# Performance work log

Hardware: AMD Instinct MI355X
Metric: run time of the kernel (lower is better)

## Reference

```python
import jax, jax.numpy as jnp
import numpy as np

B, T, D, H, O, E = 4, 2048, 1024, 2048, 1024, 8
EPS = 1e-12  # torch F.normalize p=1 eps


def setup_inputs() -> dict:
    key = jax.random.key(0)
    ks = jax.random.split(key, 8)
    s = lambda *dims: 1.0 / np.sqrt(dims[0])
    return {
        "x": jax.random.normal(ks[0], (B, T, D), dtype=jnp.float32),
        "num_experts_chosen": 2,
        "W_gate": jax.random.normal(ks[1], (D, E), dtype=jnp.float32) * s(D),
        "b_gate": jnp.zeros((E,), dtype=jnp.float32),
        "W1": jax.random.normal(ks[2], (E, D, H), dtype=jnp.float32) * s(D),
        "b1": jnp.zeros((E, H), dtype=jnp.float32),
        "W2": jax.random.normal(ks[3], (E, H, O), dtype=jnp.float32) * s(H),
        "b2": jnp.zeros((E, O), dtype=jnp.float32),
    }


def reference(x, num_experts_chosen, W_gate, b_gate, W1, b1, W2, b2):
    # Router: softmax over experts -> [b, t, E]
    gating = jax.nn.softmax(jnp.einsum("btd,de->bte", x, W_gate) + b_gate, axis=-1)

    # Top-k mask (scatter of ones at top-k indices), then L1 renormalize
    _, topk_idx = jax.lax.top_k(gating, num_experts_chosen)  # [b, t, k]
    mask = jax.nn.one_hot(topk_idx, E, dtype=gating.dtype).sum(axis=-2)  # [b, t, E]
    g = gating * mask
    g = g / jnp.maximum(jnp.sum(jnp.abs(g), axis=-1, keepdims=True), EPS)

    # Dense compute of ALL experts (faithful to original), eval-mode dropout = identity
    h = jax.nn.relu(jnp.einsum("btd,edh->bteh", x, W1) + b1)  # [b, t, E, H]
    eo = jnp.einsum("bteh,eho->bteo", h, W2) + b2              # [b, t, E, O]

    # Weighted combine over experts
    return jnp.einsum("bte,bteo->bto", g, eo)
```

## Files before the change

### kernel.cpp

```cpp
#include <hip/hip_runtime.h>
#include <hip/hip_bf16.h>

typedef unsigned short u16;
typedef __attribute__((ext_vector_type(8))) short short8;
typedef __attribute__((ext_vector_type(4))) float floatx4;

#define NB 4
#define NT 2048
#define ND 1024
#define NH 2048
#define NO 1024
#define NE 8
#define NTOK (NB * NT)

#define BM 128
#define BN 128
#define BK 32

__device__ __forceinline__ u16 f2bf(float f) {
  __hip_bfloat16 h = __float2bfloat16(f);
  return *reinterpret_cast<u16*>(&h);
}

__device__ __forceinline__ float bf2f(unsigned u) {
  return __uint_as_float(u << 16);
}

__device__ __forceinline__ void async16(const u16* g, u16* l) {
  __builtin_amdgcn_global_load_lds(
      (const __attribute__((address_space(1))) void*)g,
      (__attribute__((address_space(3))) void*)l, 16, 0, 0);
}

__global__ __launch_bounds__(256) void transpose_cvt(
    const float* __restrict__ in, u16* __restrict__ out, int R, int C) {
  __shared__ float tile[64][65];
  int e = blockIdx.z;
  in  += (size_t)e * R * C;
  out += (size_t)e * R * C;
  int c0 = blockIdx.x * 64, r0 = blockIdx.y * 64;
  int t = threadIdx.x;
#pragma unroll
  for (int i = 0; i < 4; ++i) {
    int idx = t + i * 256;
    int r = idx >> 4, cq = idx & 15;
    float4 v = *(const float4*)&in[(size_t)(r0 + r) * C + c0 + cq * 4];
    tile[r][cq * 4 + 0] = v.x; tile[r][cq * 4 + 1] = v.y;
    tile[r][cq * 4 + 2] = v.z; tile[r][cq * 4 + 3] = v.w;
  }
  __syncthreads();
#pragma unroll
  for (int i = 0; i < 4; ++i) {
    int idx = t + i * 256;
    int c = idx >> 4, rq = idx & 15;
    uint2 p;
    p.x = (unsigned)f2bf(tile[rq * 4 + 0][c]) | ((unsigned)f2bf(tile[rq * 4 + 1][c]) << 16);
    p.y = (unsigned)f2bf(tile[rq * 4 + 2][c]) | ((unsigned)f2bf(tile[rq * 4 + 3][c]) << 16);
    *(uint2*)&out[(size_t)(c0 + c) * R + r0 + rq * 4] = p;
  }
}

__global__ __launch_bounds__(256) void router_kernel(
    const float* __restrict__ x, const float* __restrict__ Wg,
    const float* __restrict__ bg, u16* __restrict__ xbf,
    int* __restrict__ counts, int* __restrict__ entries,
    float* __restrict__ wts) {
  __shared__ int   se0[32], se1[32];
  __shared__ float sw0[32], sw1[32];
  int t = threadIdx.x;
  int tl = t >> 3;
  int l8 = t & 7;
  int tok = blockIdx.x * 32 + tl;

  const float* xrow = x + (size_t)tok * ND;
  u16* xbrow = xbf + (size_t)tok * ND;
  float acc[8] = {};
#pragma unroll 4
  for (int i = 0; i < 32; ++i) {
    int d0 = l8 * 4 + i * 32;
    float4 xv = *(const float4*)&xrow[d0];
    uint2 p;
    p.x = (unsigned)f2bf(xv.x) | ((unsigned)f2bf(xv.y) << 16);
    p.y = (unsigned)f2bf(xv.z) | ((unsigned)f2bf(xv.w) << 16);
    *(uint2*)&xbrow[d0] = p;
    const float* wr = Wg + (size_t)d0 * NE;
#pragma unroll
    for (int j = 0; j < 4; ++j) {
      float xs = (j == 0) ? xv.x : (j == 1) ? xv.y : (j == 2) ? xv.z : xv.w;
      float4 w0 = *(const float4*)&wr[j * NE];
      float4 w1 = *(const float4*)&wr[j * NE + 4];
      acc[0] += xs * w0.x; acc[1] += xs * w0.y;
      acc[2] += xs * w0.z; acc[3] += xs * w0.w;
      acc[4] += xs * w1.x; acc[5] += xs * w1.y;
      acc[6] += xs * w1.z; acc[7] += xs * w1.w;
    }
  }
#pragma unroll
  for (int off = 4; off; off >>= 1)
#pragma unroll
    for (int k = 0; k < 8; ++k) acc[k] += __shfl_down(acc[k], off, 8);

  if (l8 == 0) {
    float best = -1e30f, second = -1e30f;
    int e0 = 0, e1 = 0;
#pragma unroll
    for (int i = 0; i < NE; ++i) {
      float L = acc[i] + bg[i];
      if (L > best) { second = best; e1 = e0; best = L; e0 = i; }
      else if (L > second) { second = L; e1 = i; }
    }
    float p1 = __expf(second - best);
    float inv = 1.f / (1.f + p1);
    se0[tl] = e0; se1[tl] = e1;
    sw0[tl] = inv; sw1[tl] = p1 * inv;
  }
  __syncthreads();

  if (t < NE) {
    int e = t;
    int c = 0;
#pragma unroll
    for (int k = 0; k < 32; ++k) c += (se0[k] == e) + (se1[k] == e);
    int pos = atomicAdd(&counts[e * 32], c);
    int base = blockIdx.x * 32;
    for (int k = 0; k < 32; ++k) {
      if (se0[k] == e) { entries[e * NTOK + pos] = (base + k) * 2;     wts[e * NTOK + pos] = sw0[k]; ++pos; }
      if (se1[k] == e) { entries[e * NTOK + pos] = (base + k) * 2 + 1; wts[e * NTOK + pos] = sw1[k]; ++pos; }
    }
  }
}

__global__ __launch_bounds__(256) void gemm1_kernel(
    const u16* __restrict__ xbf, const u16* __restrict__ w1t,
    const float* __restrict__ b1, const int* __restrict__ counts,
    const int* __restrict__ entries, u16* __restrict__ hbuf) {
  int b = blockIdx.x;
  int e = b & 7;
  int r = b >> 3;
  int mIdx = r >> 4;
  int n0 = (r & 15) * BN;
  int cnt = counts[e * 32];

  __shared__ u16 As[BM * BK];
  __shared__ u16 Bs[BN * BK];
  __shared__ int ent_s[BM];

  int t = threadIdx.x;
  int lane = t & 63, wv = t >> 6;
  int rl0 = wv * 32 + (lane >> 2);
  int rl1 = rl0 + 16;
  int pg = (((lane & 3) ^ ((rl0 >> 1) & 3))) * 8;
  const u16* Bbase = w1t + (size_t)e * NH * ND + (size_t)n0 * ND;
  const u16* gB0 = Bbase + (size_t)rl0 * ND + pg;
  const u16* gB1 = Bbase + (size_t)rl1 * ND + pg;
  u16* lA0 = As + (wv * 32) * BK;
  u16* lA1 = As + (wv * 32 + 16) * BK;
  u16* lB0 = Bs + (wv * 32) * BK;
  u16* lB1 = Bs + (wv * 32 + 16) * BK;

  int waveM = (wv >> 1) * 64, waveN = (wv & 1) * 64;
  int rA = lane & 15, quad = lane >> 4;
  int cR = (quad ^ ((rA >> 1) & 3)) * 8;
  const short8* aP[4]; const short8* bP[4];
#pragma unroll
  for (int i = 0; i < 4; ++i) {
    aP[i] = (const short8*)&As[(waveM + i * 16 + rA) * BK + cR];
    bP[i] = (const short8*)&Bs[(waveN + i * 16 + rA) * BK + cR];
  }

  for (int m0 = mIdx * BM; m0 < cnt; m0 += 16 * BM) {
    int rem = cnt - m0; if (rem > BM) rem = BM;
    if (t < BM) ent_s[t] = (t < rem) ? entries[e * NTOK + m0 + t] : entries[e * NTOK];
    __syncthreads();

    const u16* gA0 = xbf + (size_t)(ent_s[rl0] >> 1) * ND + pg;
    const u16* gA1 = xbf + (size_t)(ent_s[rl1] >> 1) * ND + pg;

    floatx4 acc[4][4] = {};
    for (int k0 = 0; k0 < ND; k0 += BK) {
      async16(gA0 + k0, lA0);
      async16(gA1 + k0, lA1);
      async16(gB0 + k0, lB0);
      async16(gB1 + k0, lB1);
      __syncthreads();
      short8 a[4], bb[4];
#pragma unroll
      for (int i = 0; i < 4; ++i) { a[i] = *aP[i]; bb[i] = *bP[i]; }
#pragma unroll
      for (int i = 0; i < 4; ++i)
#pragma unroll
        for (int j = 0; j < 4; ++j)
          acc[i][j] = __builtin_amdgcn_mfma_f32_16x16x32_bf16(a[i], bb[j], acc[i][j], 0, 0, 0);
      __syncthreads();
    }

#pragma unroll
    for (int i = 0; i < 4; ++i)
#pragma unroll
      for (int rr = 0; rr < 4; ++rr) {
        int lm = waveM + i * 16 + quad * 4 + rr;
        if (lm >= rem) continue;
        int ent = ent_s[lm];
        u16* dst = hbuf + (size_t)ent * NH + n0;
#pragma unroll
        for (int j = 0; j < 4; ++j) {
          int col = waveN + j * 16 + rA;
          float v = acc[i][j][rr] + b1[e * NH + n0 + col];
          dst[col] = f2bf(fmaxf(v, 0.f));
        }
      }
    __syncthreads();
  }
}

__global__ __launch_bounds__(256) void gemm2_kernel(
    const u16* __restrict__ hbuf, const u16* __restrict__ w2t,
    const float* __restrict__ b2, const int* __restrict__ counts,
    const int* __restrict__ entries, const float* __restrict__ wts,
    u16* __restrict__ eo) {
  int b = blockIdx.x;
  int e = b & 7;
  int r = b >> 3;
  int mIdx = r >> 3;
  int n0 = (r & 7) * BN;
  int cnt = counts[e * 32];

  __shared__ u16 As[BM * BK];
  __shared__ u16 Bs[BN * BK];
  __shared__ int ent_s[BM];
  __shared__ float w_s[BM];

  int t = threadIdx.x;
  int lane = t & 63, wv = t >> 6;
  int rl0 = wv * 32 + (lane >> 2);
  int rl1 = rl0 + 16;
  int pg = (((lane & 3) ^ ((rl0 >> 1) & 3))) * 8;
  const u16* Bbase = w2t + (size_t)e * NO * NH + (size_t)n0 * NH;
  const u16* gB0 = Bbase + (size_t)rl0 * NH + pg;
  const u16* gB1 = Bbase + (size_t)rl1 * NH + pg;
  u16* lA0 = As + (wv * 32) * BK;
  u16* lA1 = As + (wv * 32 + 16) * BK;
  u16* lB0 = Bs + (wv * 32) * BK;
  u16* lB1 = Bs + (wv * 32 + 16) * BK;

  int waveM = (wv >> 1) * 64, waveN = (wv & 1) * 64;
  int rA = lane & 15, quad = lane >> 4;
  int cR = (quad ^ ((rA >> 1) & 3)) * 8;
  const short8* aP[4]; const short8* bP[4];
#pragma unroll
  for (int i = 0; i < 4; ++i) {
    aP[i] = (const short8*)&As[(waveM + i * 16 + rA) * BK + cR];
    bP[i] = (const short8*)&Bs[(waveN + i * 16 + rA) * BK + cR];
  }

  for (int m0 = mIdx * BM; m0 < cnt; m0 += 16 * BM) {
    int rem = cnt - m0; if (rem > BM) rem = BM;
    if (t < BM) {
      int src = (t < rem) ? (e * NTOK + m0 + t) : (e * NTOK);
      ent_s[t] = entries[src];
      w_s[t] = wts[src];
    }
    __syncthreads();

    const u16* gA0 = hbuf + (size_t)ent_s[rl0] * NH + pg;
    const u16* gA1 = hbuf + (size_t)ent_s[rl1] * NH + pg;

    floatx4 acc[4][4] = {};
    for (int k0 = 0; k0 < NH; k0 += BK) {
      async16(gA0 + k0, lA0);
      async16(gA1 + k0, lA1);
      async16(gB0 + k0, lB0);
      async16(gB1 + k0, lB1);
      __syncthreads();
      short8 a[4], bb[4];
#pragma unroll
      for (int i = 0; i < 4; ++i) { a[i] = *aP[i]; bb[i] = *bP[i]; }
#pragma unroll
      for (int i = 0; i < 4; ++i)
#pragma unroll
        for (int j = 0; j < 4; ++j)
          acc[i][j] = __builtin_amdgcn_mfma_f32_16x16x32_bf16(a[i], bb[j], acc[i][j], 0, 0, 0);
      __syncthreads();
    }

#pragma unroll
    for (int i = 0; i < 4; ++i)
#pragma unroll
      for (int rr = 0; rr < 4; ++rr) {
        int lm = waveM + i * 16 + quad * 4 + rr;
        if (lm >= rem) continue;
        int ent = ent_s[lm];
        float w = w_s[lm];
        u16* dst = eo + (size_t)ent * NO + n0;
#pragma unroll
        for (int j = 0; j < 4; ++j) {
          int col = waveN + j * 16 + rA;
          float v = (acc[i][j][rr] + b2[e * NO + n0 + col]) * w;
          dst[col] = f2bf(v);
        }
      }
    __syncthreads();
  }
}

__global__ __launch_bounds__(256) void combine_kernel(
    const u16* __restrict__ eo, float* __restrict__ out) {
  size_t idx = (size_t)blockIdx.x * 256 + threadIdx.x;
  size_t tok = idx >> 8;
  int oq = (int)(idx & 255) * 4;
  const u16* p0 = eo + (tok * 2) * NO + oq;
  const u16* p1 = p0 + NO;
  uint2 ua = *(const uint2*)p0;
  uint2 ub = *(const uint2*)p1;
  float4 o;
  o.x = bf2f(ua.x & 0xffff) + bf2f(ub.x & 0xffff);
  o.y = bf2f(ua.x >> 16)    + bf2f(ub.x >> 16);
  o.z = bf2f(ua.y & 0xffff) + bf2f(ub.y & 0xffff);
  o.w = bf2f(ua.y >> 16)    + bf2f(ub.y >> 16);
  *(float4*)&out[tok * NO + oq] = o;
}

extern "C" void kernel_launch(void* const* d_in, const int* in_sizes, int n_in,
                              void* d_out, int out_size, void* d_ws, size_t ws_size,
                              hipStream_t stream) {
  (void)in_sizes; (void)n_in; (void)out_size; (void)ws_size;
  const float* x  = (const float*)d_in[0];
  const float* Wg = (const float*)d_in[2];
  const float* bg = (const float*)d_in[3];
  const float* W1 = (const float*)d_in[4];
  const float* b1 = (const float*)d_in[5];
  const float* W2 = (const float*)d_in[6];
  const float* b2 = (const float*)d_in[7];
  float* out = (float*)d_out;

  char* ws = (char*)d_ws;
  size_t off = 0;
  int*   counts  = (int*)(ws + off);   off += NE * 32 * 4;
  int*   entries = (int*)(ws + off);   off += (size_t)NE * NTOK * 4;
  float* wts     = (float*)(ws + off); off += (size_t)NE * NTOK * 4;
  u16*   xbf     = (u16*)(ws + off);   off += (size_t)NTOK * ND * 2;
  u16*   w1t     = (u16*)(ws + off);   off += (size_t)NE * NH * ND * 2;
  u16*   w2t     = (u16*)(ws + off);   off += (size_t)NE * NO * NH * 2;
  u16*   hbuf    = (u16*)(ws + off);   off += (size_t)NTOK * 2 * NH * 2;
  u16*   eo      = w1t;

  hipMemsetAsync(counts, 0, NE * 32 * 4, stream);

  transpose_cvt<<<dim3(NH / 64, ND / 64, NE), 256, 0, stream>>>(W1, w1t, ND, NH);
  transpose_cvt<<<dim3(NO / 64, NH / 64, NE), 256, 0, stream>>>(W2, w2t, NH, NO);
  router_kernel<<<NTOK / 32, 256, 0, stream>>>(x, Wg, bg, xbf, counts, entries, wts);
  gemm1_kernel<<<NE * 16 * (NH / BN), 256, 0, stream>>>(xbf, w1t, b1, counts, entries, hbuf);
  gemm2_kernel<<<NE * 16 * (NO / BN), 256, 0, stream>>>(hbuf, w2t, b2, counts, entries, wts, eo);
  combine_kernel<<<(NTOK * NO / 4) / 256, 256, 0, stream>>>(eo, out);
}
```

Baseline: 502.9 us.

## Double GEMM K-tile to 64 with 8-way LDS swizzle and fuse prep kernels

Raises BK from 32 to 64 in both expert GEMMs. Each k-step now loads four 16-byte async chunks per operand per thread and issues two MFMA k-substeps, which halves the number of barrier pairs per tile. It also changes the LDS XOR swizzle to 8 chunks to match the wider rows. Separately, the router and both weight transpose/convert kernels are merged into one prep kernel launch so they can overlap and launch overhead drops. The cost is double the LDS per block, which may lower occupancy, and a larger shared tile allocation in every prep block.

After: 456.8 us. -9.2%, faster.

```diff
diff --git a/kernel.cpp b/kernel.cpp
--- a/kernel.cpp
+++ b/kernel.cpp
@@ -15,7 +15,11 @@
 
 #define BM 128
 #define BN 128
-#define BK 32
+#define BK 64
+
+#define RTR_BLKS (NTOK / 32)
+#define T1_BLKS  ((NH / 64) * (ND / 64) * NE)
+#define T2_BLKS  ((NO / 64) * (NH / 64) * NE)
 
 __device__ __forceinline__ u16 f2bf(float f) {
   __hip_bfloat16 h = __float2bfloat16(f);
@@ -32,13 +36,12 @@
       (__attribute__((address_space(3))) void*)l, 16, 0, 0);
 }
 
-__global__ __launch_bounds__(256) void transpose_cvt(
-    const float* __restrict__ in, u16* __restrict__ out, int R, int C) {
-  __shared__ float tile[64][65];
-  int e = blockIdx.z;
+__device__ __forceinline__ void transpose_body(
+    const float* __restrict__ in, u16* __restrict__ out, int R, int C,
+    int bx, int by, int e, float (*tile)[65]) {
   in  += (size_t)e * R * C;
   out += (size_t)e * R * C;
-  int c0 = blockIdx.x * 64, r0 = blockIdx.y * 64;
+  int c0 = bx * 64, r0 = by * 64;
   int t = threadIdx.x;
 #pragma unroll
   for (int i = 0; i < 4; ++i) {
@@ -60,17 +63,37 @@
   }
 }
 
-__global__ __launch_bounds__(256) void router_kernel(
+__global__ __launch_bounds__(256) void prep_kernel(
     const float* __restrict__ x, const float* __restrict__ Wg,
     const float* __restrict__ bg, u16* __restrict__ xbf,
     int* __restrict__ counts, int* __restrict__ entries,
-    float* __restrict__ wts) {
+    float* __restrict__ wts,
+    const float* __restrict__ W1, u16* __restrict__ w1t,
+    const float* __restrict__ W2, u16* __restrict__ w2t) {
+  __shared__ float tile[64][65];
   __shared__ int   se0[32], se1[32];
   __shared__ float sw0[32], sw1[32];
+  int b = blockIdx.x;
+
+  if (b >= RTR_BLKS) {
+    int lb = b - RTR_BLKS;
+    if (lb < T1_BLKS) {
+      int e = lb >> 9;
+      int rem = lb & 511;
+      transpose_body(W1, w1t, ND, NH, rem & 31, rem >> 5, e, tile);
+    } else {
+      int lb2 = lb - T1_BLKS;
+      int e = lb2 >> 9;
+      int rem = lb2 & 511;
+      transpose_body(W2, w2t, NH, NO, rem & 15, rem >> 4, e, tile);
+    }
+    return;
+  }
+
   int t = threadIdx.x;
   int tl = t >> 3;
   int l8 = t & 7;
-  int tok = blockIdx.x * 32 + tl;
+  int tok = b * 32 + tl;
 
   const float* xrow = x + (size_t)tok * ND;
   u16* xbrow = xbf + (size_t)tok * ND;
@@ -122,7 +145,7 @@
 #pragma unroll
     for (int k = 0; k < 32; ++k) c += (se0[k] == e) + (se1[k] == e);
     int pos = atomicAdd(&counts[e * 32], c);
-    int base = blockIdx.x * 32;
+    int base = b * 32;
     for (int k = 0; k < 32; ++k) {
       if (se0[k] == e) { entries[e * NTOK + pos] = (base + k) * 2;     wts[e * NTOK + pos] = sw0[k]; ++pos; }
       if (se1[k] == e) { entries[e * NTOK + pos] = (base + k) * 2 + 1; wts[e * NTOK + pos] = sw1[k]; ++pos; }
@@ -147,50 +170,54 @@
 
   int t = threadIdx.x;
   int lane = t & 63, wv = t >> 6;
-  int rl0 = wv * 32 + (lane >> 2);
-  int rl1 = rl0 + 16;
-  int pg = (((lane & 3) ^ ((rl0 >> 1) & 3))) * 8;
+  int srow = lane >> 3;
+  int sc   = ((lane & 7) ^ (srow & 7)) * 8;
   const u16* Bbase = w1t + (size_t)e * NH * ND + (size_t)n0 * ND;
-  const u16* gB0 = Bbase + (size_t)rl0 * ND + pg;
-  const u16* gB1 = Bbase + (size_t)rl1 * ND + pg;
-  u16* lA0 = As + (wv * 32) * BK;
-  u16* lA1 = As + (wv * 32 + 16) * BK;
-  u16* lB0 = Bs + (wv * 32) * BK;
-  u16* lB1 = Bs + (wv * 32 + 16) * BK;
+  const u16* gB[4];
+  u16* lA[4]; u16* lB[4];
+#pragma unroll
+  for (int d = 0; d < 4; ++d) {
+    int rowl = wv * 32 + d * 8;
+    gB[d] = Bbase + (size_t)(rowl + srow) * ND + sc;
+    lA[d] = As + rowl * BK;
+    lB[d] = Bs + rowl * BK;
+  }
 
   int waveM = (wv >> 1) * 64, waveN = (wv & 1) * 64;
   int rA = lane & 15, quad = lane >> 4;
-  int cR = (quad ^ ((rA >> 1) & 3)) * 8;
-  const short8* aP[4]; const short8* bP[4];
-#pragma unroll
-  for (int i = 0; i < 4; ++i) {
-    aP[i] = (const short8*)&As[(waveM + i * 16 + rA) * BK + cR];
-    bP[i] = (const short8*)&Bs[(waveN + i * 16 + rA) * BK + cR];
-  }
+  int ch0 = ((quad) ^ (rA & 7)) * 8;
+  int ch1 = ((quad + 4) ^ (rA & 7)) * 8;
 
   for (int m0 = mIdx * BM; m0 < cnt; m0 += 16 * BM) {
     int rem = cnt - m0; if (rem > BM) rem = BM;
     if (t < BM) ent_s[t] = (t < rem) ? entries[e * NTOK + m0 + t] : entries[e * NTOK];
     __syncthreads();
 
-    const u16* gA0 = xbf + (size_t)(ent_s[rl0] >> 1) * ND + pg;
-    const u16* gA1 = xbf + (size_t)(ent_s[rl1] >> 1) * ND + pg;
+    const u16* gA[4];
+#pragma unroll
+    for (int d = 0; d < 4; ++d)
+      gA[d] = xbf + (size_t)(ent_s[wv * 32 + d * 8 + srow] >> 1) * ND + sc;
 
     floatx4 acc[4][4] = {};
     for (int k0 = 0; k0 < ND; k0 += BK) {
-      async16(gA0 + k0, lA0);
-      async16(gA1 + k0, lA1);
-      async16(gB0 + k0, lB0);
-      async16(gB1 + k0, lB1);
+#pragma unroll
+      for (int d = 0; d < 4; ++d) { async16(gA[d] + k0, lA[d]); async16(gB[d] + k0, lB[d]); }
       __syncthreads();
-      short8 a[4], bb[4];
-#pragma unroll
-      for (int i = 0; i < 4; ++i) { a[i] = *aP[i]; bb[i] = *bP[i]; }
-#pragma unroll
-      for (int i = 0; i < 4; ++i)
-#pragma unroll
-        for (int j = 0; j < 4; ++j)
-          acc[i][j] = __builtin_amdgcn_mfma_f32_16x16x32_bf16(a[i], bb[j], acc[i][j], 0, 0, 0);
+      short8 a[2][4], bb[2][4];
+#pragma unroll
+      for (int i = 0; i < 4; ++i) {
+        const u16* ar = As + (waveM + i * 16 + rA) * BK;
+        const u16* br = Bs + (waveN + i * 16 + rA) * BK;
+        a[0][i] = *(const short8*)(ar + ch0);  a[1][i] = *(const short8*)(ar + ch1);
+        bb[0][i] = *(const short8*)(br + ch0); bb[1][i] = *(const short8*)(br + ch1);
+      }
+#pragma unroll
+      for (int kk = 0; kk < 2; ++kk)
+#pragma unroll
+        for (int i = 0; i < 4; ++i)
+#pragma unroll
+          for (int j = 0; j < 4; ++j)
+            acc[i][j] = __builtin_amdgcn_mfma_f32_16x16x32_bf16(a[kk][i], bb[kk][j], acc[i][j], 0, 0, 0);
       __syncthreads();
     }
 
@@ -232,26 +259,23 @@
 
   int t = threadIdx.x;
   int lane = t & 63, wv = t >> 6;
-  int rl0 = wv * 32 + (lane >> 2);
-  int rl1 = rl0 + 16;
-  int pg = (((lane & 3) ^ ((rl0 >> 1) & 3))) * 8;
+  int srow = lane >> 3;
+  int sc   = ((lane & 7) ^ (srow & 7)) * 8;
   const u16* Bbase = w2t + (size_t)e * NO * NH + (size_t)n0 * NH;
-  const u16* gB0 = Bbase + (size_t)rl0 * NH + pg;
-  const u16* gB1 = Bbase + (size_t)rl1 * NH + pg;
-  u16* lA0 = As + (wv * 32) * BK;
-  u16* lA1 = As + (wv * 32 + 16) * BK;
-  u16* lB0 = Bs + (wv * 32) * BK;
-  u16* lB1 = Bs + (wv * 32 + 16) * BK;
+  const u16* gB[4];
+  u16* lA[4]; u16* lB[4];
+#pragma unroll
+  for (int d = 0; d < 4; ++d) {
+    int rowl = wv * 32 + d * 8;
+    gB[d] = Bbase + (size_t)(rowl + srow) * NH + sc;
+    lA[d] = As + rowl * BK;
+    lB[d] = Bs + rowl * BK;
+  }
 
   int waveM = (wv >> 1) * 64, waveN = (wv & 1) * 64;
   int rA = lane & 15, quad = lane >> 4;
-  int cR = (quad ^ ((rA >> 1) & 3)) * 8;
-  const short8* aP[4]; const short8* bP[4];
-#pragma unroll
-  for (int i = 0; i < 4; ++i) {
-    aP[i] = (const short8*)&As[(waveM + i * 16 + rA) * BK + cR];
-    bP[i] = (const short8*)&Bs[(waveN + i * 16 + rA) * BK + cR];
-  }
+  int ch0 = ((quad) ^ (rA & 7)) * 8;
+  int ch1 = ((quad + 4) ^ (rA & 7)) * 8;
 
   for (int m0 = mIdx * BM; m0 < cnt; m0 += 16 * BM) {
     int rem = cnt - m0; if (rem > BM) rem = BM;
@@ -262,24 +286,31 @@
     }
     __syncthreads();
 
-    const u16* gA0 = hbuf + (size_t)ent_s[rl0] * NH + pg;
-    const u16* gA1 = hbuf + (size_t)ent_s[rl1] * NH + pg;
+    const u16* gA[4];
+#pragma unroll
+    for (int d = 0; d < 4; ++d)
+      gA[d] = hbuf + (size_t)ent_s[wv * 32 + d * 8 + srow] * NH + sc;
 
     floatx4 acc[4][4] = {};
     for (int k0 = 0; k0 < NH; k0 += BK) {
-      async16(gA0 + k0, lA0);
-      async16(gA1 + k0, lA1);
-      async16(gB0 + k0, lB0);
-      async16(gB1 + k0, lB1);
+#pragma unroll
+      for (int d = 0; d < 4; ++d) { async16(gA[d] + k0, lA[d]); async16(gB[d] + k0, lB[d]); }
       __syncthreads();
-      short8 a[4], bb[4];
-#pragma unroll
-      for (int i = 0; i < 4; ++i) { a[i] = *aP[i]; bb[i] = *bP[i]; }
-#pragma unroll
-      for (int i = 0; i < 4; ++i)
-#pragma unroll
-        for (int j = 0; j < 4; ++j)
-          acc[i][j] = __builtin_amdgcn_mfma_f32_16x16x32_bf16(a[i], bb[j], acc[i][j], 0, 0, 0);
+      short8 a[2][4], bb[2][4];
+#pragma unroll
+      for (int i = 0; i < 4; ++i) {
+        const u16* ar = As + (waveM + i * 16 + rA) * BK;
+        const u16* br = Bs + (waveN + i * 16 + rA) * BK;
+        a[0][i] = *(const short8*)(ar + ch0);  a[1][i] = *(const short8*)(ar + ch1);
+        bb[0][i] = *(const short8*)(br + ch0); bb[1][i] = *(const short8*)(br + ch1);
+      }
+#pragma unroll
+      for (int kk = 0; kk < 2; ++kk)
+#pragma unroll
+        for (int i = 0; i < 4; ++i)
+#pragma unroll
+          for (int j = 0; j < 4; ++j)
+            acc[i][j] = __builtin_amdgcn_mfma_f32_16x16x32_bf16(a[kk][i], bb[kk][j], acc[i][j], 0, 0, 0);
       __syncthreads();
     }
 
@@ -346,9 +377,8 @@
 
   hipMemsetAsync(counts, 0, NE * 32 * 4, stream);
 
-  transpose_cvt<<<dim3(NH / 64, ND / 64, NE), 256, 0, stream>>>(W1, w1t, ND, NH);
-  transpose_cvt<<<dim3(NO / 64, NH / 64, NE), 256, 0, stream>>>(W2, w2t, NH, NO);
-  router_kernel<<<NTOK / 32, 256, 0, stream>>>(x, Wg, bg, xbf, counts, entries, wts);
+  prep_kernel<<<RTR_BLKS + T1_BLKS + T2_BLKS, 256, 0, stream>>>(
+      x, Wg, bg, xbf, counts, entries, wts, W1, w1t, W2, w2t);
   gemm1_kernel<<<NE * 16 * (NH / BN), 256, 0, stream>>>(xbf, w1t, b1, counts, entries, hbuf);
   gemm2_kernel<<<NE * 16 * (NO / BN), 256, 0, stream>>>(hbuf, w2t, b2, counts, entries, wts, eo);
   combine_kernel<<<(NTOK * NO / 4) / 256, 256, 0, stream>>>(eo, out);
```
